# Performance work log

Measured on AMD Instinct MI355X. Metric: run time of the kernel, lower is better.

Reference implementation:

```python
import jax, jax.numpy as jnp
import numpy as np

DIM = 1024
HEADS = 16
DIM_HEAD = 64
INNER = HEADS * DIM_HEAD  # 1024
SCALE = DIM_HEAD ** -0.5


def layernorm(x, gamma, beta, eps=1e-5):
    mu = jnp.mean(x, axis=-1, keepdims=True)
    var = jnp.var(x, axis=-1, keepdims=True)
    return (x - mu) * jax.lax.rsqrt(var + eps) * gamma + beta


def setup_inputs() -> dict:
    key = jax.random.key(0)
    ks = jax.random.split(key, 6)
    x = jax.random.normal(ks[0], (2, 2048, DIM), dtype=jnp.float32)
    # params (stored [in, out]; torch Linear does x @ W.T with W [out, in])
    w_q = jax.random.normal(ks[1], (DIM, INNER), dtype=jnp.float32) * (DIM ** -0.5)
    w_kv = jax.random.normal(ks[2], (DIM, 2 * INNER), dtype=jnp.float32) * (DIM ** -0.5)
    w_out = jax.random.normal(ks[3], (INNER, DIM), dtype=jnp.float32) * (INNER ** -0.5)
    b_out = jnp.zeros((DIM,), dtype=jnp.float32)
    gamma = jnp.ones((DIM,), dtype=jnp.float32)
    beta = jnp.zeros((DIM,), dtype=jnp.float32)
    return {"x": x, "w_q": w_q, "w_kv": w_kv, "w_out": w_out, "b_out": b_out,
            "gamma": gamma, "beta": beta}


def reference(x, w_q, w_kv, w_out, b_out, gamma, beta):
    b, n, _ = x.shape
    xn = layernorm(x, gamma, beta)
    q = xn @ w_q                           # [b, n, inner]
    kv = xn @ w_kv                         # [b, n, 2*inner]
    k, v = jnp.split(kv, 2, axis=-1)
    def split_heads(t):
        return t.reshape(b, n, HEADS, DIM_HEAD).transpose(0, 2, 1, 3)  # b h n d
    q, k, v = split_heads(q), split_heads(k), split_heads(v)
    dots = jnp.einsum('bhid,bhjd->bhij', q, k) * SCALE   # [b, h, n, n]
    attn = jax.nn.softmax(dots, axis=-1)
    out = jnp.einsum('bhij,bhjd->bhid', attn, v)          # [b, h, n, d]
    out = out.transpose(0, 2, 1, 3).reshape(b, n, INNER)  # b n (h d)
    return out @ w_out + b_out
```

## Files before the change

kernel.cpp:

```cpp
#include <hip/hip_runtime.h>

typedef unsigned short u16;
typedef u16   u16x8 __attribute__((ext_vector_type(8)));
typedef __bf16 bf16x8 __attribute__((ext_vector_type(8)));
typedef float f32x4 __attribute__((ext_vector_type(4)));
typedef float f32x2 __attribute__((ext_vector_type(2)));
typedef _Float16 f16x4 __attribute__((ext_vector_type(4)));
typedef _Float16 f16x8 __attribute__((ext_vector_type(8)));
typedef unsigned u32x2 __attribute__((ext_vector_type(2)));
typedef unsigned u32x4 __attribute__((ext_vector_type(4)));

__device__ __forceinline__ u16 f2b(float f){ __bf16 h=(__bf16)f; return __builtin_bit_cast(u16,h); }

__device__ __forceinline__ float ex2(float x){
#if __has_builtin(__builtin_amdgcn_exp2f)
  return __builtin_amdgcn_exp2f(x);
#else
  float r; asm("v_exp_f32 %0, %1" : "=v"(r) : "v"(x)); return r;
#endif
}

__device__ __forceinline__ f32x4 mfma16(u16x8 a, u16x8 b, f32x4 c){
  return __builtin_amdgcn_mfma_f32_16x16x32_bf16(
      __builtin_bit_cast(bf16x8,a), __builtin_bit_cast(bf16x8,b), c, 0,0,0);
}

__device__ __forceinline__ f32x4 mfma32h(f16x8 a, f16x8 b, f32x4 c){
  return __builtin_amdgcn_mfma_f32_16x16x32_f16(a, b, c, 0,0,0);
}

__device__ __forceinline__ void gl2lds16(const u16* g, u16* l){
  __builtin_amdgcn_global_load_lds((const __attribute__((address_space(1))) void*)g,
                                   (__attribute__((address_space(3))) void*)l, 16, 0, 0);
}

__global__ __launch_bounds__(256) void ln_kernel(const float* __restrict__ x,
                                                 const float* __restrict__ gamma,
                                                 const float* __restrict__ beta,
                                                 u16* __restrict__ xn){
  const int row = blockIdx.x, t = threadIdx.x;
  const float4 v = ((const float4*)(x + (size_t)row*1024))[t];
  float s  = v.x+v.y+v.z+v.w;
  float sq = v.x*v.x+v.y*v.y+v.z*v.z+v.w*v.w;
  for (int m=1;m<64;m<<=1){ s += __shfl_xor(s,m); sq += __shfl_xor(sq,m); }
  __shared__ float red[8];
  const int w=t>>6, l=t&63;
  if(l==0){ red[w]=s; red[4+w]=sq; }
  __syncthreads();
  const float S  = red[0]+red[1]+red[2]+red[3];
  const float SQ = red[4]+red[5]+red[6]+red[7];
  const float mu = S*(1.f/1024.f);
  const float var= SQ*(1.f/1024.f)-mu*mu;
  const float rs = rsqrtf(var+1e-5f);
  const float4 g4=((const float4*)gamma)[t], b4=((const float4*)beta)[t];
  u16 o0=f2b((v.x-mu)*rs*g4.x+b4.x);
  u16 o1=f2b((v.y-mu)*rs*g4.y+b4.y);
  u16 o2=f2b((v.z-mu)*rs*g4.z+b4.z);
  u16 o3=f2b((v.w-mu)*rs*g4.w+b4.w);
  uint2 p; p.x=(unsigned)o0|((unsigned)o1<<16); p.y=(unsigned)o2|((unsigned)o3<<16);
  ((uint2*)(xn + (size_t)row*1024))[t]=p;
}

__global__ __launch_bounds__(256) void wtrans_all_kernel(const float* __restrict__ wq,
    const float* __restrict__ wkv, const float* __restrict__ wout,
    u16* __restrict__ wqkvt, u16* __restrict__ woutt){
  __shared__ float tile[64][65];
  const int bx=blockIdx.x, t=threadIdx.x;
  const float* in; u16* out; int C, cxx;
  if(bx<16){ in=wq;  out=wqkvt;           C=1024; cxx=bx; }
  else if(bx<48){ in=wkv; out=wqkvt+1024*1024; C=2048; cxx=bx-16; }
  else { in=wout; out=woutt;             C=1024; cxx=bx-48; }
  const int R=1024;
  const int c0=cxx*64, r0=blockIdx.y*64;
  {
    const int r=t>>2, cc=t&3;
    const float* gp = in + (size_t)(r0+r)*C + c0 + cc*16;
    #pragma unroll
    for(int i=0;i<4;i++){
      float4 f=((const float4*)gp)[i];
      tile[r][cc*16+i*4+0]=f.x; tile[r][cc*16+i*4+1]=f.y;
      tile[r][cc*16+i*4+2]=f.z; tile[r][cc*16+i*4+3]=f.w;
    }
  }
  __syncthreads();
  const int c=t>>2, rc=t&3;
  u16x8 a,b;
  #pragma unroll
  for(int i=0;i<8;i++) a[i]=f2b(tile[rc*16+i][c]);
  #pragma unroll
  for(int i=0;i<8;i++) b[i]=f2b(tile[rc*16+8+i][c]);
  u16* op = out + (size_t)(c0+c)*R + r0 + rc*16;
  *(u16x8*)op=a; *(u16x8*)(op+8)=b;
}

template<int MODE,int TM>
__global__ __launch_bounds__(256) void gemm_bt_kernel(const u16* __restrict__ A,
    const u16* __restrict__ Bt, u16* __restrict__ outQ, u16* __restrict__ outK,
    u16* __restrict__ outV, float* __restrict__ outF, const float* __restrict__ bias,
    float scale, int M, int N, int K){
  constexpr int MT = TM/32;
  __shared__ u16 As[TM*64];
  __shared__ u16 Bs[128*64];
  const int t=threadIdx.x, w=t>>6, l=t&63, qd=l>>4, ln=l&15;
  const int m0=blockIdx.y*TM, n0=blockIdx.x*128;
  const int wm=(w>>1)*(TM/2), wn=(w&1)*64;
  f32x4 acc[MT][4] = {};
  const int nK = K>>6;
  for(int kt=0; kt<nK; kt++){
    const int k0=kt*64;
    #pragma unroll
    for(int p=0;p<MT;p++){
      const int cid=p*256+t, r=cid>>3, pc=cid&7, g=pc^(r&7);
      gl2lds16(A + (size_t)(m0+r)*K + k0 + g*8, &As[(p*256 + (t&192))*8]);
    }
    #pragma unroll
    for(int p=0;p<4;p++){
      const int cid=p*256+t, r=cid>>3, pc=cid&7, g=pc^(r&7);
      gl2lds16(Bt + (size_t)(n0+r)*K + k0 + g*8, &Bs[(p*256 + (t&192))*8]);
    }
    __syncthreads();
    #pragma unroll
    for(int ks=0;ks<2;ks++){
      u16x8 af[MT], bf[4];
      #pragma unroll
      for(int mt=0;mt<MT;mt++){
        const int m=wm+mt*16+ln, kc=ks*4+qd, pcc=kc^(m&7);
        af[mt]=*(const u16x8*)&As[m*64 + pcc*8];
      }
      #pragma unroll
      for(int nt=0;nt<4;nt++){
        const int n=wn+nt*16+ln, kc=ks*4+qd, pcc=kc^(n&7);
        bf[nt]=*(const u16x8*)&Bs[n*64 + pcc*8];
      }
      #pragma unroll
      for(int mt=0;mt<MT;mt++)
        #pragma unroll
        for(int nt=0;nt<4;nt++)
          acc[mt][nt]=mfma16(af[mt],bf[nt],acc[mt][nt]);
    }
    __syncthreads();
  }
  if(MODE==1){
    #pragma unroll
    for(int mt=0;mt<MT;mt++)
      #pragma unroll
      for(int rr=0;rr<4;rr++){
        const int row = m0+wm+mt*16+qd*4+rr;
        #pragma unroll
        for(int nt=0;nt<4;nt++){
          const int col = n0+wn+nt*16+ln;
          outF[(size_t)row*N+col]=acc[mt][nt][rr]+bias[col];
        }
      }
  } else if(n0<1024){
    #pragma unroll
    for(int mt=0;mt<MT;mt++)
      #pragma unroll
      for(int rr=0;rr<4;rr++){
        const int row = m0+wm+mt*16+qd*4+rr;
        #pragma unroll
        for(int nt=0;nt<4;nt++)
          outQ[(size_t)row*1024 + n0+wn+nt*16+ln]=f2b(acc[mt][nt][rr]*scale);
      }
  } else if(n0<2048){
    u16* kp = outK + (size_t)((m0>>11)*16 + ((n0-1024+wn)>>6))*131072;
    const int jb = (m0&2047) + wm;
    #pragma unroll
    for(int mt=0;mt<MT;mt++)
      #pragma unroll
      for(int rr=0;rr<4;rr++){
        const int j = jb + mt*16 + qd*4 + rr;
        #pragma unroll
        for(int nt=0;nt<4;nt++)
          kp[(size_t)j*64 + nt*16+ln]=f2b(acc[mt][nt][rr]);
      }
  } else {
    u16* vpp = outV + (size_t)((m0>>11)*16 + ((n0-2048+wn)>>6))*131072;
    const int jb = (m0&2047) + wm;
    #pragma unroll
    for(int mt=0;mt<MT;mt++){
      const int j = jb + mt*16 + qd*4;
      const int grp = (j>>5)*4 + ((j>>3)&3);
      const int sub = j&7;
      #pragma unroll
      for(int nt=0;nt<4;nt++){
        const auto lo=__builtin_amdgcn_cvt_pkrtz(acc[mt][nt][0],acc[mt][nt][1]);
        const auto hi=__builtin_amdgcn_cvt_pkrtz(acc[mt][nt][2],acc[mt][nt][3]);
        uint2 w2; w2.x=__builtin_bit_cast(unsigned,lo); w2.y=__builtin_bit_cast(unsigned,hi);
        *(uint2*)&vpp[(size_t)(grp*64 + nt*16+ln)*8 + sub] = w2;
      }
    }
  }
}

__global__ __launch_bounds__(512,4) void attn_kernel(const u16* __restrict__ Q,
    const u16* __restrict__ Kp, const u16* __restrict__ Vp, u16* __restrict__ O){
  __shared__ u16 Ks[2][8192];
  __shared__ u16 Vs[2][8192];
  const int qt=blockIdx.x, h=blockIdx.y, bb=blockIdx.z;
  const int t=threadIdx.x, w=t>>6, l=t&63, qd=l>>4, ln=l&15;
  const int q0=qt*128;
  const size_t baseQ=(size_t)bb*2048*1024 + h*64;
  const size_t baseKV=(size_t)(bb*16+h)*131072;
  u16x8 qf[2];
  #pragma unroll
  for(int ks=0;ks<2;ks++)
    qf[ks] = *(const u16x8*)(Q + baseQ + (size_t)(q0+w*16+ln)*1024 + ks*32+qd*8);
  f32x4 o_acc[4]={};
  f32x4 l_acc={};
  const f16x8 onesB={(_Float16)1.f,(_Float16)1.f,(_Float16)1.f,(_Float16)1.f,
                     (_Float16)1.f,(_Float16)1.f,(_Float16)1.f,(_Float16)1.f};
  const f32x4 zf={0.f,0.f,0.f,0.f};

  int koff[2];
  #pragma unroll
  for(int p=0;p<2;p++){
    const int r=(p*512+t)>>3, g=(t&7)^(r&7);
    const int pr=(r&~31)+((r>>2)&3)*8+((r>>4)&1)*4+(r&3);
    koff[p]=pr*64+g*8;
  }

  auto stage=[&](int buf,int j0){
    #pragma unroll
    for(int p=0;p<2;p++)
      gl2lds16(Kp + baseKV + (size_t)j0*64 + koff[p], &Ks[buf][(p*512+(t&448))*8]);
    #pragma unroll
    for(int p=0;p<2;p++)
      gl2lds16(Vp + baseKV + (size_t)(j0>>5)*2048 + (size_t)(p*512+t)*8,
               &Vs[buf][(p*512+(t&448))*8]);
  };

  stage(0,0);
  __syncthreads();
  int cur=0;
  for(int jt=0;jt<16;jt++){
    if(jt<15) stage(cur^1,(jt+1)*128);
    const u16* Kb=&Ks[cur][0];
    const u16* Vb=&Vs[cur][0];
    #pragma unroll
    for(int jh=0;jh<2;jh++){
      f16x8 vall[2][4];
      #pragma unroll
      for(int al=0;al<2;al++)
        #pragma unroll
        for(int dt=0;dt<4;dt++)
          vall[al][dt]=*(const f16x8*)&Vb[(((jh*2+al)*4+qd)*64 + dt*16+ln)*8];
      f32x4 s[4];
      #pragma unroll
      for(int ks=0;ks<2;ks++){
        u16x8 kf[4];
        #pragma unroll
        for(int j4=0;j4<4;j4++){
          const int row=(jh*4+j4)*16+ln;
          kf[j4]=*(const u16x8*)&Kb[row*64 + (((ks*4+qd)^(ln&7))*8)];
        }
        __builtin_amdgcn_s_setprio(1);
        #pragma unroll
        for(int j4=0;j4<4;j4++)
          s[j4] = ks? mfma16(kf[j4],qf[1],s[j4]) : mfma16(kf[j4],qf[0],zf);
        __builtin_amdgcn_s_setprio(0);
      }
      #pragma unroll
      for(int al=0;al<2;al++){
        const int t0=al*2, t1=al*2+1;
        u32x4 pw;
        pw.x=__builtin_bit_cast(unsigned,__builtin_amdgcn_cvt_pkrtz(ex2(s[t0][0]),ex2(s[t0][1])));
        pw.y=__builtin_bit_cast(unsigned,__builtin_amdgcn_cvt_pkrtz(ex2(s[t0][2]),ex2(s[t0][3])));
        pw.z=__builtin_bit_cast(unsigned,__builtin_amdgcn_cvt_pkrtz(ex2(s[t1][0]),ex2(s[t1][1])));
        pw.w=__builtin_bit_cast(unsigned,__builtin_amdgcn_cvt_pkrtz(ex2(s[t1][2]),ex2(s[t1][3])));
        const f16x8 pf=__builtin_bit_cast(f16x8,pw);
        __builtin_amdgcn_s_setprio(1);
        l_acc=mfma32h(pf,onesB,l_acc);
        #pragma unroll
        for(int dt=0;dt<4;dt++)
          o_acc[dt]=mfma32h(pf,vall[al][dt],o_acc[dt]);
        __builtin_amdgcn_s_setprio(0);
      }
    }
    __syncthreads();
    cur^=1;
  }

  #pragma unroll
  for(int rr=0;rr<4;rr++){
    const float lr=1.f/l_acc[rr];
    const int row=q0+w*16+qd*4+rr;
    #pragma unroll
    for(int dt=0;dt<4;dt++)
      O[baseQ + (size_t)row*1024 + dt*16+ln]=f2b(o_acc[dt][rr]*lr);
  }
}

extern "C" void kernel_launch(void* const* d_in, const int* in_sizes, int n_in,
                              void* d_out, int out_size, void* d_ws, size_t ws_size,
                              hipStream_t stream) {
  const float* x     = (const float*)d_in[0];
  const float* w_q   = (const float*)d_in[1];
  const float* w_kv  = (const float*)d_in[2];
  const float* w_out = (const float*)d_in[3];
  const float* b_out = (const float*)d_in[4];
  const float* gamma = (const float*)d_in[5];
  const float* beta  = (const float*)d_in[6];
  float* out = (float*)d_out;

  char* ws=(char*)d_ws;
  size_t off=0;
  u16* xn    =(u16*)(ws+off); off += (size_t)4096*1024*2;
  u16* wqkvt =(u16*)(ws+off); off += (size_t)3072*1024*2;
  u16* woutt =(u16*)(ws+off); off += (size_t)1024*1024*2;
  u16* qb    =(u16*)(ws+off); off += (size_t)4096*1024*2;
  u16* kpb   =(u16*)(ws+off); off += (size_t)4096*1024*2;
  u16* vpb   =(u16*)(ws+off); off += (size_t)4096*1024*2;
  u16* ob    =(u16*)(ws+off); off += (size_t)4096*1024*2;

  ln_kernel<<<4096,256,0,stream>>>(x,gamma,beta,xn);
  wtrans_all_kernel<<<dim3(64,16),256,0,stream>>>(w_q,w_kv,w_out,wqkvt,woutt);

  const float SCALE_Q = 0.125f*1.4426950408889634f;
  gemm_bt_kernel<2,128><<<dim3(24,32),256,0,stream>>>(xn,wqkvt,qb,kpb,vpb,nullptr,nullptr,SCALE_Q,4096,3072,1024);
  attn_kernel<<<dim3(16,16,2),512,0,stream>>>(qb,kpb,vpb,ob);
  gemm_bt_kernel<1,128><<<dim3(8,32),256,0,stream>>>(ob,woutt,nullptr,nullptr,nullptr,out,b_out,1.f,4096,1024,1024);
}
```

Before: 195.9 us.

## Software-pipeline QK^T with softmax/PV across half-tiles; shrink out-proj GEMM tile

Restructures the attention inner loop so the QK^T MFMAs for the next 64-key half-tile are issued before the exp/PV work of the previous half-tile. This lets matrix-core work overlap the transcendental and conversion work, and the barrier and next-stage prefetch are moved between the halves. It also changes the output-projection GEMM to a 64-row tile variant with twice as many blocks, to improve occupancy and load balance. The change raises register pressure from the extra live score and V fragments, and the smaller GEMM tile reduces data reuse.

```diff
diff --git a/kernel.cpp b/kernel.cpp
--- a/kernel.cpp
+++ b/kernel.cpp
@@ -230,56 +230,112 @@
                &Vs[buf][(p*512+(t&448))*8]);
   };
 
+  auto qk0=[&](const int buf, f32x4 (&sN)[4]){
+    const u16* Kb=&Ks[buf][0];
+    #pragma unroll
+    for(int ks=0;ks<2;ks++){
+      u16x8 kf[4];
+      #pragma unroll
+      for(int j4=0;j4<4;j4++)
+        kf[j4]=*(const u16x8*)&Kb[(j4*16+ln)*64 + (((ks*4+qd)^(ln&7))*8)];
+      __builtin_amdgcn_s_setprio(1);
+      #pragma unroll
+      for(int j4=0;j4<4;j4++)
+        sN[j4] = ks? mfma16(kf[j4],qf[1],sN[j4]) : mfma16(kf[j4],qf[0],zf);
+      __builtin_amdgcn_s_setprio(0);
+    }
+  };
+  auto qk1=[&](const int buf, f32x4 (&sN)[4], f16x8 (&vN)[2][4]){
+    const u16* Kb=&Ks[buf][0];
+    const u16* Vb=&Vs[buf][0];
+    #pragma unroll
+    for(int al=0;al<2;al++)
+      #pragma unroll
+      for(int dt=0;dt<4;dt++)
+        vN[al][dt]=*(const f16x8*)&Vb[(((2+al)*4+qd)*64 + dt*16+ln)*8];
+    #pragma unroll
+    for(int ks=0;ks<2;ks++){
+      u16x8 kf[4];
+      #pragma unroll
+      for(int j4=0;j4<4;j4++)
+        kf[j4]=*(const u16x8*)&Kb[((4+j4)*16+ln)*64 + (((ks*4+qd)^(ln&7))*8)];
+      __builtin_amdgcn_s_setprio(1);
+      #pragma unroll
+      for(int j4=0;j4<4;j4++)
+        sN[j4] = ks? mfma16(kf[j4],qf[1],sN[j4]) : mfma16(kf[j4],qf[0],zf);
+      __builtin_amdgcn_s_setprio(0);
+    }
+  };
+  auto sm_pv_reg=[&](f32x4 (&s)[4], f16x8 (&vv)[2][4]){
+    #pragma unroll
+    for(int al=0;al<2;al++){
+      const int t0=al*2, t1=al*2+1;
+      u32x4 pw;
+      pw.x=__builtin_bit_cast(unsigned,__builtin_amdgcn_cvt_pkrtz(ex2(s[t0][0]),ex2(s[t0][1])));
+      pw.y=__builtin_bit_cast(unsigned,__builtin_amdgcn_cvt_pkrtz(ex2(s[t0][2]),ex2(s[t0][3])));
+      pw.z=__builtin_bit_cast(unsigned,__builtin_amdgcn_cvt_pkrtz(ex2(s[t1][0]),ex2(s[t1][1])));
+      pw.w=__builtin_bit_cast(unsigned,__builtin_amdgcn_cvt_pkrtz(ex2(s[t1][2]),ex2(s[t1][3])));
+      const f16x8 pf=__builtin_bit_cast(f16x8,pw);
+      __builtin_amdgcn_s_setprio(1);
+      l_acc=mfma32h(pf,onesB,l_acc);
+      #pragma unroll
+      for(int dt=0;dt<4;dt++)
+        o_acc[dt]=mfma32h(pf,vv[al][dt],o_acc[dt]);
+      __builtin_amdgcn_s_setprio(0);
+    }
+  };
+  auto sm_pv_lds=[&](f32x4 (&s)[4], const int buf){
+    const u16* Vb=&Vs[buf][0];
+    #pragma unroll
+    for(int al=0;al<2;al++){
+      f16x8 vv[4];
+      #pragma unroll
+      for(int dt=0;dt<4;dt++)
+        vv[dt]=*(const f16x8*)&Vb[((al*4+qd)*64 + dt*16+ln)*8];
+      const int t0=al*2, t1=al*2+1;
+      u32x4 pw;
+      pw.x=__builtin_bit_cast(unsigned,__builtin_amdgcn_cvt_pkrtz(ex2(s[t0][0]),ex2(s[t0][1])));
+      pw.y=__builtin_bit_cast(unsigned,__builtin_amdgcn_cvt_pkrtz(ex2(s[t0][2]),ex2(s[t0][3])));
+      pw.z=__builtin_bit_cast(unsigned,__builtin_amdgcn_cvt_pkrtz(ex2(s[t1][0]),ex2(s[t1][1])));
+      pw.w=__builtin_bit_cast(unsigned,__builtin_amdgcn_cvt_pkrtz(ex2(s[t1][2]),ex2(s[t1][3])));
+      const f16x8 pf=__builtin_bit_cast(f16x8,pw);
+      __builtin_amdgcn_s_setprio(1);
+      l_acc=mfma32h(pf,onesB,l_acc);
+      #pragma unroll
+      for(int dt=0;dt<4;dt++)
+        o_acc[dt]=mfma32h(pf,vv[dt],o_acc[dt]);
+      __builtin_amdgcn_s_setprio(0);
+    }
+  };
+
+  f32x4 sP[4];
+  f16x8 vP[2][4];
+
   stage(0,0);
   __syncthreads();
+  stage(1,128);
+  qk0(0,sP);
   int cur=0;
-  for(int jt=0;jt<16;jt++){
-    if(jt<15) stage(cur^1,(jt+1)*128);
-    const u16* Kb=&Ks[cur][0];
-    const u16* Vb=&Vs[cur][0];
-    #pragma unroll
-    for(int jh=0;jh<2;jh++){
-      f16x8 vall[2][4];
-      #pragma unroll
-      for(int al=0;al<2;al++)
-        #pragma unroll
-        for(int dt=0;dt<4;dt++)
-          vall[al][dt]=*(const f16x8*)&Vb[(((jh*2+al)*4+qd)*64 + dt*16+ln)*8];
-      f32x4 s[4];
-      #pragma unroll
-      for(int ks=0;ks<2;ks++){
-        u16x8 kf[4];
-        #pragma unroll
-        for(int j4=0;j4<4;j4++){
-          const int row=(jh*4+j4)*16+ln;
-          kf[j4]=*(const u16x8*)&Kb[row*64 + (((ks*4+qd)^(ln&7))*8)];
-        }
-        __builtin_amdgcn_s_setprio(1);
-        #pragma unroll
-        for(int j4=0;j4<4;j4++)
-          s[j4] = ks? mfma16(kf[j4],qf[1],s[j4]) : mfma16(kf[j4],qf[0],zf);
-        __builtin_amdgcn_s_setprio(0);
-      }
-      #pragma unroll
-      for(int al=0;al<2;al++){
-        const int t0=al*2, t1=al*2+1;
-        u32x4 pw;
-        pw.x=__builtin_bit_cast(unsigned,__builtin_amdgcn_cvt_pkrtz(ex2(s[t0][0]),ex2(s[t0][1])));
-        pw.y=__builtin_bit_cast(unsigned,__builtin_amdgcn_cvt_pkrtz(ex2(s[t0][2]),ex2(s[t0][3])));
-        pw.z=__builtin_bit_cast(unsigned,__builtin_amdgcn_cvt_pkrtz(ex2(s[t1][0]),ex2(s[t1][1])));
-        pw.w=__builtin_bit_cast(unsigned,__builtin_amdgcn_cvt_pkrtz(ex2(s[t1][2]),ex2(s[t1][3])));
-        const f16x8 pf=__builtin_bit_cast(f16x8,pw);
-        __builtin_amdgcn_s_setprio(1);
-        l_acc=mfma32h(pf,onesB,l_acc);
-        #pragma unroll
-        for(int dt=0;dt<4;dt++)
-          o_acc[dt]=mfma32h(pf,vall[al][dt],o_acc[dt]);
-        __builtin_amdgcn_s_setprio(0);
-      }
-    }
-    __syncthreads();
-    cur^=1;
-  }
+  for(int tile=0;tile<16;tile++){
+    {
+      f32x4 sN[4];
+      qk1(cur,sN,vP);
+      sm_pv_lds(sP,cur);
+      #pragma unroll
+      for(int i=0;i<4;i++) sP[i]=sN[i];
+    }
+    if(tile<15){
+      __syncthreads();
+      cur^=1;
+      if(tile<14) stage(cur^1,(tile+2)*128);
+      f32x4 sN[4];
+      qk0(cur,sN);
+      sm_pv_reg(sP,vP);
+      #pragma unroll
+      for(int i=0;i<4;i++) sP[i]=sN[i];
+    }
+  }
+  sm_pv_reg(sP,vP);
 
   #pragma unroll
   for(int rr=0;rr<4;rr++){
@@ -319,5 +375,5 @@
   const float SCALE_Q = 0.125f*1.4426950408889634f;
   gemm_bt_kernel<2,128><<<dim3(24,32),256,0,stream>>>(xn,wqkvt,qb,kpb,vpb,nullptr,nullptr,SCALE_Q,4096,3072,1024);
   attn_kernel<<<dim3(16,16,2),512,0,stream>>>(qb,kpb,vpb,ob);
-  gemm_bt_kernel<1,128><<<dim3(8,32),256,0,stream>>>(ob,woutt,nullptr,nullptr,nullptr,out,b_out,1.f,4096,1024,1024);
-}
+  gemm_bt_kernel<1,64><<<dim3(8,64),256,0,stream>>>(ob,woutt,nullptr,nullptr,nullptr,out,b_out,1.f,4096,1024,1024);
+}
```

Result: faster. 179.4 us (-8.5%).
